# Optimization experiments

Measured on AMD Instinct MI355X. Metric: run time of the kernel, lower is better.

## Reference

```python
import jax, jax.numpy as jnp
import numpy as np

STRIDES = (8, 16, 32)
INPUT = (640, 640)
NC = 80           # num_classes
CONF = 0.65       # conf_thr
IOU_THR = 0.65    # nms iou_threshold
K = 1000          # fixed candidate cap for jit-compatible NMS (padded/masked)


def _priors():
    # MlvlPointGenerator(offset=0, with_stride=True): per level, points at
    # (x*stride, y*stride) flattened y-major, format [cx, cy, stride, stride].
    ps = []
    for s in STRIDES:
        H, W = INPUT[0] // s, INPUT[1] // s
        yy, xx = jnp.meshgrid(jnp.arange(H, dtype=jnp.float32),
                              jnp.arange(W, dtype=jnp.float32), indexing='ij')
        cx = (xx * s).ravel()
        cy = (yy * s).ravel()
        st = jnp.full_like(cx, float(s))
        ps.append(jnp.stack([cx, cy, st, st], axis=-1))
    return jnp.concatenate(ps, axis=0)  # [8400, 4]


def _flatten(xs, c):
    # permute(0,2,3,1).reshape(B, -1, c) per level, concat over priors
    return jnp.concatenate(
        [x.transpose(0, 2, 3, 1).reshape(x.shape[0], -1, c) for x in xs], axis=1)


def _decode(priors, bp):
    # bp: [B, N, 4]; priors: [N, 4] (cx, cy, sw, sh)
    xys = bp[..., :2] * priors[:, 2:] + priors[:, :2]
    whs = jnp.exp(bp[..., 2:]) * priors[:, 2:]
    tl = xys - whs * 0.5
    br = xys + whs * 0.5
    return jnp.concatenate([tl, br], axis=-1)  # [B, N, 4] tlbr


def _iou(a, b):
    tl = jnp.maximum(a[:, None, :2], b[None, :, :2])
    br = jnp.minimum(a[:, None, 2:], b[None, :, 2:])
    wh = jnp.clip(br - tl, 0.0)
    inter = wh[..., 0] * wh[..., 1]
    area = lambda x: (x[:, 2] - x[:, 0]) * (x[:, 3] - x[:, 1])
    union = area(a)[:, None] + area(b)[None, :] - inter
    return inter / (union + 1e-6)


def _nms_single(cls_s, obj_s, boxes):
    # cls_s: [N, NC] sigmoid scores; obj_s: [N]; boxes: [N, 4]
    max_s = cls_s.max(axis=-1)
    labels = jnp.argmax(cls_s, axis=-1)
    score = max_s * obj_s
    valid = score >= CONF                       # confidence mask
    sc = jnp.where(valid, score, 0.0)
    top_sc, idx = jax.lax.top_k(sc, K)          # sorted descending -> greedy order
    b = boxes[idx]
    lab = labels[idx]
    v = valid[idx]
    # class-aware (batched) NMS: offset boxes per label so classes never overlap
    max_coord = jnp.max(jnp.abs(b)) + 1.0
    ob = b + (lab.astype(b.dtype) * max_coord)[:, None]
    iou = _iou(ob, ob)                          # [K, K]
    j = jnp.arange(K)
    def body(i, keep):
        sup = (iou[i] > IOU_THR) & (j > i)
        return jnp.where(keep[i] & v[i], keep & (~sup), keep)
    keep = jax.lax.fori_loop(0, K, body, jnp.ones(K, dtype=bool))
    final = keep & v
    dets = jnp.where(final[:, None],
                     jnp.concatenate([b, top_sc[:, None]], axis=-1), 0.0)  # [K, 5]
    labs = jnp.where(final, lab, -1)
    return dets, labs, final


def setup_inputs() -> dict:
    key = jax.random.key(0)
    ks = jax.random.split(key, 9)
    B = 32
    shapes = {
        'cls0': (B, NC, 80, 80), 'cls1': (B, NC, 40, 40), 'cls2': (B, NC, 20, 20),
        'bbox0': (B, 4, 80, 80), 'bbox1': (B, 4, 40, 40), 'bbox2': (B, 4, 20, 20),
        'obj0': (B, 1, 80, 80), 'obj1': (B, 1, 40, 40), 'obj2': (B, 1, 20, 20),
    }
    return {n: jax.random.normal(k, s, dtype=jnp.float32)
            for (n, s), k in zip(shapes.items(), ks)}


def reference(cls0, cls1, cls2, bbox0, bbox1, bbox2, obj0, obj1, obj2):
    priors = _priors()
    cls = jax.nn.sigmoid(_flatten([cls0, cls1, cls2], NC))       # [B, 8400, 80]
    bp = _flatten([bbox0, bbox1, bbox2], 4)                      # [B, 8400, 4]
    obj = jax.nn.sigmoid(_flatten([obj0, obj1, obj2], 1)[..., 0])  # [B, 8400]
    boxes = _decode(priors, bp)                                  # [B, 8400, 4]
    # per-image class-wise batched NMS, padded to K detections
    dets, labels, keep = jax.vmap(_nms_single)(cls, obj, boxes)
    return dets, labels, keep
```

## Files before the change

### kernel.cpp

```cpp
#include <hip/hip_runtime.h>
#include <stdint.h>

#define NPRIOR 8400
#define NB 32
#define NCLS 80
#define KTOP 1000
#define CAP 8400
#define CPAD 16

typedef unsigned long long u64;

__device__ __forceinline__ float exp_np(float x) {
#pragma clang fp contract(off)
    if (x > 88.72283935546875f) return __builtin_huge_valf();
    if (x < -87.3365478515625f) return 0.0f;
    float q = rintf(x * 1.442695040f);
    float r = fmaf(q, -6.93145752e-1f, x);
    r = fmaf(q, -1.42860677e-6f, r);
    float p = fmaf(1.9875691500e-4f, r, 1.3981999507e-3f);
    p = fmaf(p, r, 8.3334519073e-3f);
    p = fmaf(p, r, 4.1665795894e-2f);
    p = fmaf(p, r, 1.6666665459e-1f);
    p = fmaf(p, r, 5.0000001201e-1f);
    float r2 = r * r;
    p = fmaf(p, r2, r);
    p = p + 1.0f;
    return ldexpf(p, (int)q);
}
__device__ __forceinline__ float sigm_np(float x) {
#pragma clang fp contract(off)
    float t = exp_np(-x);
    return 1.0f / (1.0f + t);
}

__device__ __forceinline__ void level_of(int n, int& W, int& s, int& loc) {
    if (n < 6400)      { W = 80; s = 8;  loc = n; }
    else if (n < 8000) { W = 40; s = 16; loc = n - 6400; }
    else               { W = 20; s = 32; loc = n - 8000; }
}

__device__ float4 decode32(int b, int n,
                           const float* bb0, const float* bb1, const float* bb2) {
#pragma clang fp contract(off)
    int W, s, loc; level_of(n, W, s, loc);
    const float* bb = (s == 8) ? bb0 : (s == 16) ? bb1 : bb2;
    int hw = W * W;
    int y = loc / W, x = loc - y * W;
    const float* bp = bb + (size_t)b * 4 * hw + y * W + x;
    float fs = (float)s;
    float cx = (float)x * fs, cy = (float)y * fs;
    float xc = bp[0] * fs + cx;
    float yc = bp[hw] * fs + cy;
    float wv = exp_np(bp[2 * hw]) * fs;
    float hv = exp_np(bp[3 * hw]) * fs;
    float wv2 = wv * 0.5f, hv2 = hv * 0.5f;
    float4 r;
    r.x = xc - wv2;
    r.y = yc - hv2;
    r.z = xc + wv2;
    r.w = yc + hv2;
    return r;
}

__global__ void __launch_bounds__(64) init_k(int* __restrict__ cnts_mb) {
    cnts_mb[threadIdx.x * CPAD] = 0;
}

__global__ void __launch_bounds__(256) score_k(
    const float* __restrict__ cls0, const float* __restrict__ cls1, const float* __restrict__ cls2,
    const float* __restrict__ ob0,  const float* __restrict__ ob1,  const float* __restrict__ ob2,
    float* __restrict__ sc, int* __restrict__ labels,
    u64* __restrict__ keys, int* __restrict__ cnts, int* __restrict__ rankbuf)
{
#pragma clang fp contract(off)
    int b = blockIdx.y;
    int n = blockIdx.x * 256 + threadIdx.x;
    bool nvalid = (n < NPRIOR);
    int nc = nvalid ? n : NPRIOR - 1;
    int W, s, loc; level_of(nc, W, s, loc);
    const float* cls = (s == 8) ? cls0 : (s == 16) ? cls1 : cls2;
    const float* ob  = (s == 8) ? ob0  : (s == 16) ? ob1  : ob2;
    int hw = W * W;
    int y = loc / W, x = loc - y * W;
    const float* cp = cls + (size_t)b * NCLS * hw + y * W + x;

    float M = -3.4e38f, S2 = -3.4e38f;
    int I = 0;
    for (int cb = 0; cb < NCLS; cb += 8) {
        float buf[8];
#pragma unroll
        for (int k = 0; k < 8; ++k) buf[k] = cp[(size_t)(cb + k) * hw];
#pragma unroll
        for (int k = 0; k < 8; ++k) {
            float l = buf[k];
            if (l > M) { S2 = M; M = l; I = cb + k; }
            else       { S2 = fmaxf(S2, l); }
        }
    }

    float tM = sigm_np(M);
    int lab = I;
    float gap = M - S2;
    float mx = fmaxf(fabsf(M), fabsf(S2));
    if (!((gap * exp_np(-mx)) > 1.6e-5f)) {
        tM = -1.0f; lab = 0;
        for (int c = 0; c < NCLS; ++c) {
            float t = sigm_np(cp[(size_t)c * hw]);
            if (t > tM) { tM = t; lab = c; }
        }
    }
    float sObj = sigm_np(ob[(size_t)b * hw + y * W + x]);
    float score = tM * sObj;
    float scv = (score >= 0.65f) ? score : 0.0f;
    if (nvalid) {
        sc[(size_t)b * NPRIOR + n] = scv;
        labels[(size_t)b * NPRIOR + n] = lab;
    }

    int lane = threadIdx.x & 63;
    bool val = nvalid && (scv > 0.0f);
    u64 mb = __ballot(val);
    if (mb) {
        int lead = (int)__builtin_ctzll(mb);
        int base = 0;
        if (lane == lead) base = atomicAdd(&cnts[b * CPAD], (int)__popcll(mb));
        base = __shfl(base, lead);
        if (val) {
            int pos = base + (int)__popcll(mb & ((1ull << lane) - 1ull));
            keys[(size_t)b * CAP + pos] =
                ((u64)__float_as_uint(scv) << 32) | (unsigned)(~(unsigned)n);
            rankbuf[(size_t)b * CAP + pos] = 0;
        }
    }
}

__global__ void __launch_bounds__(256) rank_part(
    const u64* __restrict__ keys, const int* __restrict__ cnts,
    int* __restrict__ rankbuf)
{
    int b = blockIdx.y, tid = threadIdx.x;
    int cn = min(cnts[b * CPAD], CAP);
    int nt = (cn + 255) >> 8;
    int ntt = nt * nt;
    const u64* keyimg = keys + (size_t)b * CAP;
    int lane = tid & 63;

    for (int t = blockIdx.x; t < ntt; t += gridDim.x) {
        int it = t / nt, jt = t - it * nt;
        int i = it * 256 + tid;
        u64 ki = (i < cn) ? keyimg[i] : ~0ull;
        int rank = 0;
        int jbase = jt * 256;
        int jend = min(jbase + 256, cn);
        for (int jb = jbase; jb < jend; jb += 64) {
            int j = jb + lane;
            u64 kv = (j < cn) ? keyimg[j] : 0ull;
            unsigned lo = (unsigned)kv, hi = (unsigned)(kv >> 32);
            int lim = jend - jb;
#pragma unroll
            for (int l = 0; l < 64; ++l) {
                unsigned jlo = __builtin_amdgcn_readlane(lo, l);
                unsigned jhi = __builtin_amdgcn_readlane(hi, l);
                u64 kj = ((u64)jhi << 32) | jlo;
                rank += (l < lim && kj > ki) ? 1 : 0;
            }
        }
        if (i < cn && rank > 0) atomicAdd(&rankbuf[(size_t)b * CAP + i], rank);
    }
}

__global__ void __launch_bounds__(256) scatter_k(
    const u64* __restrict__ keys, const int* __restrict__ cnts,
    const int* __restrict__ rankbuf,
    const float* __restrict__ sc, const int* __restrict__ labels,
    const float* __restrict__ bb0, const float* __restrict__ bb1, const float* __restrict__ bb2,
    float4* __restrict__ sel_box, float* __restrict__ sel_score,
    int* __restrict__ sel_label, int* __restrict__ maxbits, u64* __restrict__ vmask)
{
#pragma clang fp contract(off)
    __shared__ float redbuf[256];
    int b = blockIdx.y, chunk = blockIdx.x, tid = threadIdx.x;
    int cn = min(cnts[b * CPAD], CAP);
    int base = chunk * 256;
    if (chunk != 0 && base >= cn) return;

    const u64* keyimg = keys + (size_t)b * CAP;
    const int* labb = labels + (size_t)b * NPRIOR;
    const float* scb = sc + (size_t)b * NPRIOR;

    int i = base + tid;
    float lmax = 0.0f;
    if (i < cn) {
        int rank = rankbuf[(size_t)b * CAP + i];
        if (rank < KTOP) {
            u64 ki = keyimg[i];
            unsigned n = ~(unsigned)(ki & 0xffffffffull);
            float s = __uint_as_float((unsigned)(ki >> 32));
            float4 bx = decode32(b, (int)n, bb0, bb1, bb2);
            sel_box[(size_t)b * 1024 + rank] = bx;
            sel_score[(size_t)b * 1024 + rank] = s;
            sel_label[(size_t)b * 1024 + rank] = labb[n];
            lmax = fmaxf(fmaxf(fabsf(bx.x), fabsf(bx.y)),
                         fmaxf(fabsf(bx.z), fabsf(bx.w)));
        }
    }

    if (chunk == 0) {
        if (cn < KTOP && tid == 0) {
            float lm = 0.0f;
            int r = cn;
            for (int n = 0; n < NPRIOR && r < KTOP; ++n) {
                if (scb[n] == 0.0f) {
                    float4 bx = decode32(b, n, bb0, bb1, bb2);
                    sel_box[(size_t)b * 1024 + r] = bx;
                    sel_score[(size_t)b * 1024 + r] = 0.0f;
                    sel_label[(size_t)b * 1024 + r] = labb[n];
                    lm = fmaxf(lm, fmaxf(fmaxf(fabsf(bx.x), fabsf(bx.y)),
                                         fmaxf(fabsf(bx.z), fabsf(bx.w))));
                    ++r;
                }
            }
            lmax = fmaxf(lmax, lm);
        }
        if (tid < 24) {
            sel_box[(size_t)b * 1024 + 1000 + tid] = make_float4(0.f, 0.f, 0.f, 0.f);
            sel_score[(size_t)b * 1024 + 1000 + tid] = 0.0f;
            sel_label[(size_t)b * 1024 + 1000 + tid] = 0;
        }
        if (tid < 16) {
            int vc = min(cn, KTOP);
            int lo = tid * 64;
            u64 m;
            if (vc >= lo + 64)      m = ~0ull;
            else if (vc <= lo)      m = 0ull;
            else                    m = (1ull << (vc - lo)) - 1ull;
            vmask[b * 16 + tid] = m;
        }
    }

    redbuf[tid] = lmax;
    __syncthreads();
    for (int off = 128; off > 0; off >>= 1) {
        if (tid < off) redbuf[tid] = fmaxf(redbuf[tid], redbuf[tid + off]);
        __syncthreads();
    }
    if (tid == 0) atomicMax(&maxbits[b * CPAD], __float_as_int(redbuf[0]));
}

__global__ void __launch_bounds__(256) build_mask_T(
    const float4* __restrict__ sel_box, const int* __restrict__ sel_label,
    const int* __restrict__ maxbits, u64* __restrict__ Cmask)
{
#pragma clang fp contract(off)
    __shared__ float4 obr[256];
    __shared__ float arr[256];
    int b = blockIdx.y;
    int cg = blockIdx.x & 15, rgq = blockIdx.x >> 4;
    if (rgq * 4 > cg) return;
    int tid = threadIdx.x, wave = tid >> 6, lane = tid & 63;
    float mc = __int_as_float(maxbits[b * CPAD]) + 1.0f;

    {
        int row = rgq * 256 + tid;
        float4 v = sel_box[(size_t)b * 1024 + row];
        float off = (float)sel_label[(size_t)b * 1024 + row] * mc;
        v.x += off; v.y += off; v.z += off; v.w += off;
        obr[tid] = v;
        arr[tid] = (v.z - v.x) * (v.w - v.y);
    }
    int col = cg * 64 + lane;
    float4 a = sel_box[(size_t)b * 1024 + col];
    float offc = (float)sel_label[(size_t)b * 1024 + col] * mc;
    a.x += offc; a.y += offc; a.z += offc; a.w += offc;
    float ac = (a.z - a.x) * (a.w - a.y);
    __syncthreads();

    int rg = rgq * 4 + wave;
    if (rg > cg) return;
    u64 bits = 0;
    int rowbase = rg * 64;
#pragma unroll 8
    for (int r = 0; r < 64; ++r) {
        int row = rowbase + r;
        float4 rb = obr[wave * 64 + r];
        float ra = arr[wave * 64 + r];
        bool pred = false;
        if (row < col && row < KTOP && col < KTOP) {
            float tlx = fmaxf(rb.x, a.x), tly = fmaxf(rb.y, a.y);
            float brx = fminf(rb.z, a.z), bry = fminf(rb.w, a.w);
            float w = fmaxf(brx - tlx, 0.0f), h = fmaxf(bry - tly, 0.0f);
            float inter = w * h;
            float uni = (ra + ac) - inter;
            float iou = inter / (uni + 1e-6f);
            pred = iou > 0.65f;
        }
        bits |= pred ? (1ull << r) : 0ull;
    }
    Cmask[((size_t)b * 16 + rg) * 1024 + col] = bits;
}

__global__ void __launch_bounds__(64) nms_fixpoint_write(
    const u64* __restrict__ Cmask, const u64* __restrict__ vmask,
    const float4* __restrict__ sel_box, const float* __restrict__ sel_score,
    const int* __restrict__ sel_label, float* __restrict__ out)
{
    int b = blockIdx.x, lane = threadIdx.x;
    const u64* Cimg = Cmask + (size_t)b * 16 * 1024;
    u64 Khist[16];
#pragma unroll
    for (int g = 0; g < 16; ++g) {
        int col = g * 64 + lane;
        bool supp = false;
#pragma unroll
        for (int gp = 0; gp < g; ++gp)
            supp |= (Cimg[(size_t)gp * 1024 + col] & Khist[gp]) != 0ull;
        u64 V = vmask[b * 16 + g] & ~__ballot(supp);
        u64 T = Cimg[(size_t)g * 1024 + col];
        u64 K = V;
        for (int it = 0; it < 64; ++it) {
            u64 Knew = V & ~__ballot((T & K) != 0ull);
            if (Knew == K) break;
            K = Knew;
        }
        Khist[g] = K;
    }

    const size_t selo = (size_t)b * 1024;
    float* lab_o = out + (size_t)NB * KTOP * 5;
    float* keep_o = lab_o + (size_t)NB * KTOP;
#pragma unroll
    for (int g = 0; g < 16; ++g) {
        int k = g * 64 + lane;
        if (k >= KTOP) break;
        bool fin = (Khist[g] >> lane) & 1ull;
        float4 bx = sel_box[selo + k];
        float s = sel_score[selo + k];
        int lb = sel_label[selo + k];
        size_t o5 = ((size_t)b * KTOP + k) * 5;
        out[o5 + 0] = fin ? bx.x : 0.0f;
        out[o5 + 1] = fin ? bx.y : 0.0f;
        out[o5 + 2] = fin ? bx.z : 0.0f;
        out[o5 + 3] = fin ? bx.w : 0.0f;
        out[o5 + 4] = fin ? s : 0.0f;
        lab_o[b * KTOP + k] = fin ? (float)lb : -1.0f;
        keep_o[b * KTOP + k] = fin ? 1.0f : 0.0f;
    }
}

extern "C" void kernel_launch(void* const* d_in, const int* in_sizes, int n_in,
                              void* d_out, int out_size, void* d_ws, size_t ws_size,
                              hipStream_t stream) {
    const float* cls0 = (const float*)d_in[0];
    const float* cls1 = (const float*)d_in[1];
    const float* cls2 = (const float*)d_in[2];
    const float* bb0  = (const float*)d_in[3];
    const float* bb1  = (const float*)d_in[4];
    const float* bb2  = (const float*)d_in[5];
    const float* ob0  = (const float*)d_in[6];
    const float* ob1  = (const float*)d_in[7];
    const float* ob2  = (const float*)d_in[8];
    float* out = (float*)d_out;

    char* w = (char*)d_ws;
    size_t used = 0;
    auto alloc = [&](size_t bytes) -> void* {
        void* p = (void*)(w + used);
        used += (bytes + 255) & ~(size_t)255;
        return p;
    };
    float* sc        = (float*)alloc((size_t)NB * NPRIOR * 4);
    int* labels      = (int*)alloc((size_t)NB * NPRIOR * 4);
    u64* keys        = (u64*)alloc((size_t)NB * CAP * 8);
    int* cnts_mb     = (int*)alloc((size_t)2 * NB * CPAD * 4);
    int* rankbuf     = (int*)alloc((size_t)NB * CAP * 4);
    float4* sel_box  = (float4*)alloc((size_t)NB * 1024 * 16);
    float* sel_score = (float*)alloc((size_t)NB * 1024 * 4);
    int* sel_label   = (int*)alloc((size_t)NB * 1024 * 4);
    u64* vmask       = (u64*)alloc((size_t)NB * 16 * 8);
    u64* Cmask       = (u64*)alloc((size_t)NB * 16 * 1024 * 8);

    if (used > ws_size) return;

    int* cnts = cnts_mb;
    int* maxbits = cnts_mb + NB * CPAD;

    init_k<<<1, 64, 0, stream>>>(cnts_mb);
    score_k<<<dim3((NPRIOR + 255) / 256, NB), 256, 0, stream>>>(
        cls0, cls1, cls2, ob0, ob1, ob2, sc, labels, keys, cnts, rankbuf);
    rank_part<<<dim3(64, NB), 256, 0, stream>>>(keys, cnts, rankbuf);
    scatter_k<<<dim3((CAP + 255) / 256, NB), 256, 0, stream>>>(
        keys, cnts, rankbuf, sc, labels, bb0, bb1, bb2,
        sel_box, sel_score, sel_label, maxbits, vmask);
    build_mask_T<<<dim3(64, NB), 256, 0, stream>>>(sel_box, sel_label, maxbits, Cmask);
    nms_fixpoint_write<<<NB, 64, 0, stream>>>(
        Cmask, vmask, sel_box, sel_score, sel_label, out);
}
```

Before: 117.8 us.

## Split class max-reduction across 8 channel chunks with a second combine kernel

The per-prior reduction over 80 class logits is split into 8 chunks of 10 classes, each handled by its own block in a first kernel that writes a packed max/index and a second-max to workspace. A second kernel combines the partials, computes the score and does the compaction. The counter reset moves from the separate init kernel into the first kernel. This raises parallelism on the bandwidth-heavy class read (33 blocks x 32 images -> 8x more blocks), at the cost of extra partial-buffer traffic (~25 MB) and one more launch.

```diff
diff --git a/kernel.cpp b/kernel.cpp
--- a/kernel.cpp
+++ b/kernel.cpp
@@ -7,6 +7,8 @@
 #define KTOP 1000
 #define CAP 8400
 #define CPAD 16
+#define PCH 8
+#define CPC 10
 
 typedef unsigned long long u64;
 
@@ -62,47 +64,89 @@
     return r;
 }
 
-__global__ void __launch_bounds__(64) init_k(int* __restrict__ cnts_mb) {
-    cnts_mb[threadIdx.x * CPAD] = 0;
-}
-
-__global__ void __launch_bounds__(256) score_k(
+__device__ __forceinline__ unsigned flt2ord(float f) {
+    unsigned u = __float_as_uint(f);
+    return u ^ ((u >> 31) ? 0xffffffffu : 0x80000000u);
+}
+__device__ __forceinline__ float ord2flt(unsigned u) {
+    u ^= ((u >> 31) ? 0x80000000u : 0xffffffffu);
+    return __uint_as_float(u);
+}
+__device__ __forceinline__ u64 packlc(float l, int c) {
+    return ((u64)flt2ord(l) << 32) | (unsigned)(~(unsigned)c);
+}
+
+__global__ void __launch_bounds__(256) score1_k(
     const float* __restrict__ cls0, const float* __restrict__ cls1, const float* __restrict__ cls2,
-    const float* __restrict__ ob0,  const float* __restrict__ ob1,  const float* __restrict__ ob2,
+    u64* __restrict__ partP, float* __restrict__ partS, int* __restrict__ cnts_mb)
+{
+    int b = blockIdx.z, ch = blockIdx.y;
+    if (blockIdx.x == 0 && ch == 0 && threadIdx.x == 0) {
+        cnts_mb[b * CPAD] = 0;
+        cnts_mb[(NB + b) * CPAD] = 0;
+    }
+    int n = blockIdx.x * 256 + threadIdx.x;
+    if (n >= NPRIOR) return;
+    int W, s, loc; level_of(n, W, s, loc);
+    const float* cls = (s == 8) ? cls0 : (s == 16) ? cls1 : cls2;
+    int hw = W * W;
+    int y = loc / W, x = loc - y * W;
+    const float* cp = cls + (size_t)b * NCLS * hw + (size_t)(ch * CPC) * hw + y * W + x;
+
+    float buf[CPC];
+#pragma unroll
+    for (int k = 0; k < CPC; ++k) buf[k] = cp[(size_t)k * hw];
+    float M = buf[0], S2 = -3.4e38f;
+    int I = ch * CPC;
+#pragma unroll
+    for (int k = 1; k < CPC; ++k) {
+        float l = buf[k];
+        if (l > M) { S2 = M; M = l; I = ch * CPC + k; }
+        else       { S2 = fmaxf(S2, l); }
+    }
+    size_t o = ((size_t)ch * NB + b) * NPRIOR + n;
+    partP[o] = packlc(M, I);
+    partS[o] = S2;
+}
+
+__global__ void __launch_bounds__(256) score2_k(
+    const float* __restrict__ cls0, const float* __restrict__ cls1, const float* __restrict__ cls2,
+    const float* __restrict__ ob0, const float* __restrict__ ob1, const float* __restrict__ ob2,
+    const u64* __restrict__ partP, const float* __restrict__ partS,
     float* __restrict__ sc, int* __restrict__ labels,
     u64* __restrict__ keys, int* __restrict__ cnts, int* __restrict__ rankbuf)
 {
 #pragma clang fp contract(off)
     int b = blockIdx.y;
     int n = blockIdx.x * 256 + threadIdx.x;
-    bool nvalid = (n < NPRIOR);
-    int nc = nvalid ? n : NPRIOR - 1;
-    int W, s, loc; level_of(nc, W, s, loc);
+    if (n >= NPRIOR) return;
+    int W, s, loc; level_of(n, W, s, loc);
     const float* cls = (s == 8) ? cls0 : (s == 16) ? cls1 : cls2;
     const float* ob  = (s == 8) ? ob0  : (s == 16) ? ob1  : ob2;
     int hw = W * W;
     int y = loc / W, x = loc - y * W;
-    const float* cp = cls + (size_t)b * NCLS * hw + y * W + x;
-
-    float M = -3.4e38f, S2 = -3.4e38f;
-    int I = 0;
-    for (int cb = 0; cb < NCLS; cb += 8) {
-        float buf[8];
-#pragma unroll
-        for (int k = 0; k < 8; ++k) buf[k] = cp[(size_t)(cb + k) * hw];
-#pragma unroll
-        for (int k = 0; k < 8; ++k) {
-            float l = buf[k];
-            if (l > M) { S2 = M; M = l; I = cb + k; }
-            else       { S2 = fmaxf(S2, l); }
-        }
-    }
-
+
+    size_t idx = (size_t)b * NPRIOR + n;
+    const size_t cstride = (size_t)NB * NPRIOR;
+    u64 bp = partP[idx];
+    float bz = partS[idx];
+    float m2 = -3.4e38f;
+#pragma unroll
+    for (int ch = 1; ch < PCH; ++ch) {
+        u64 t = partP[(size_t)ch * cstride + idx];
+        float z = partS[(size_t)ch * cstride + idx];
+        if (t > bp) { m2 = fmaxf(m2, ord2flt((unsigned)(bp >> 32))); bp = t; bz = z; }
+        else        { m2 = fmaxf(m2, ord2flt((unsigned)(t >> 32))); }
+    }
+    m2 = fmaxf(m2, bz);
+
+    float M = ord2flt((unsigned)(bp >> 32));
+    int lab = (int)(~(unsigned)(bp & 0xffffffffull));
     float tM = sigm_np(M);
-    int lab = I;
-    float gap = M - S2;
-    float mx = fmaxf(fabsf(M), fabsf(S2));
+    float gap = M - m2;
+    float mx = fmaxf(fabsf(M), fabsf(m2));
     if (!((gap * exp_np(-mx)) > 1.6e-5f)) {
+        const float* cp = cls + (size_t)b * NCLS * hw + y * W + x;
         tM = -1.0f; lab = 0;
         for (int c = 0; c < NCLS; ++c) {
             float t = sigm_np(cp[(size_t)c * hw]);
@@ -112,13 +156,11 @@
     float sObj = sigm_np(ob[(size_t)b * hw + y * W + x]);
     float score = tM * sObj;
     float scv = (score >= 0.65f) ? score : 0.0f;
-    if (nvalid) {
-        sc[(size_t)b * NPRIOR + n] = scv;
-        labels[(size_t)b * NPRIOR + n] = lab;
-    }
+    sc[idx] = scv;
+    labels[idx] = lab;
 
     int lane = threadIdx.x & 63;
-    bool val = nvalid && (scv > 0.0f);
+    bool val = scv > 0.0f;
     u64 mb = __ballot(val);
     if (mb) {
         int lead = (int)__builtin_ctzll(mb);
@@ -370,6 +412,8 @@
     };
     float* sc        = (float*)alloc((size_t)NB * NPRIOR * 4);
     int* labels      = (int*)alloc((size_t)NB * NPRIOR * 4);
+    u64* partP       = (u64*)alloc((size_t)PCH * NB * NPRIOR * 8);
+    float* partS     = (float*)alloc((size_t)PCH * NB * NPRIOR * 4);
     u64* keys        = (u64*)alloc((size_t)NB * CAP * 8);
     int* cnts_mb     = (int*)alloc((size_t)2 * NB * CPAD * 4);
     int* rankbuf     = (int*)alloc((size_t)NB * CAP * 4);
@@ -384,9 +428,11 @@
     int* cnts = cnts_mb;
     int* maxbits = cnts_mb + NB * CPAD;
 
-    init_k<<<1, 64, 0, stream>>>(cnts_mb);
-    score_k<<<dim3((NPRIOR + 255) / 256, NB), 256, 0, stream>>>(
-        cls0, cls1, cls2, ob0, ob1, ob2, sc, labels, keys, cnts, rankbuf);
+    score1_k<<<dim3((NPRIOR + 255) / 256, PCH, NB), 256, 0, stream>>>(
+        cls0, cls1, cls2, partP, partS, cnts_mb);
+    score2_k<<<dim3((NPRIOR + 255) / 256, NB), 256, 0, stream>>>(
+        cls0, cls1, cls2, ob0, ob1, ob2, partP, partS,
+        sc, labels, keys, cnts, rankbuf);
     rank_part<<<dim3(64, NB), 256, 0, stream>>>(keys, cnts, rankbuf);
     scatter_k<<<dim3((CAP + 255) / 256, NB), 256, 0, stream>>>(
         keys, cnts, rankbuf, sc, labels, bb0, bb1, bb2,
```

Measured after the change: 127.0 us. 7.9% more time.

## Split class max-reduction across four lanes per prior with wave shuffles

Applied to the files above, without the earlier changes.

The score kernel now assigns four lanes per prior, each scanning 20 of the 80 class logits. Partial top-1 and runner-up values are merged with xor-shuffles using an order-preserving packed key, so ties resolve to the lowest class index. The goal is more memory-level parallelism and a shorter serial loop in the bandwidth-heavy class scan, which launches four times as many blocks. The cost is only 16 priors per wave, giving narrower contiguous loads per class row, plus extra shuffle work.

```diff
diff --git a/kernel.cpp b/kernel.cpp
--- a/kernel.cpp
+++ b/kernel.cpp
@@ -62,6 +62,18 @@
     return r;
 }
 
+__device__ __forceinline__ unsigned flt2ord(float f) {
+    unsigned u = __float_as_uint(f);
+    return u ^ ((u >> 31) ? 0xffffffffu : 0x80000000u);
+}
+__device__ __forceinline__ float ord2flt(unsigned u) {
+    u ^= ((u >> 31) ? 0x80000000u : 0xffffffffu);
+    return __uint_as_float(u);
+}
+__device__ __forceinline__ u64 packlc(float l, int c) {
+    return ((u64)flt2ord(l) << 32) | (unsigned)(~(unsigned)c);
+}
+
 __global__ void __launch_bounds__(64) init_k(int* __restrict__ cnts_mb) {
     cnts_mb[threadIdx.x * CPAD] = 0;
 }
@@ -74,7 +86,9 @@
 {
 #pragma clang fp contract(off)
     int b = blockIdx.y;
-    int n = blockIdx.x * 256 + threadIdx.x;
+    int tid = threadIdx.x, wv = tid >> 6, l = tid & 63;
+    int cid = l >> 4;
+    int n = blockIdx.x * 64 + wv * 16 + (l & 15);
     bool nvalid = (n < NPRIOR);
     int nc = nvalid ? n : NPRIOR - 1;
     int W, s, loc; level_of(nc, W, s, loc);
@@ -83,50 +97,73 @@
     int hw = W * W;
     int y = loc / W, x = loc - y * W;
     const float* cp = cls + (size_t)b * NCLS * hw + y * W + x;
-
-    float M = -3.4e38f, S2 = -3.4e38f;
-    int I = 0;
-    for (int cb = 0; cb < NCLS; cb += 8) {
-        float buf[8];
-#pragma unroll
-        for (int k = 0; k < 8; ++k) buf[k] = cp[(size_t)(cb + k) * hw];
-#pragma unroll
-        for (int k = 0; k < 8; ++k) {
-            float l = buf[k];
-            if (l > M) { S2 = M; M = l; I = cb + k; }
-            else       { S2 = fmaxf(S2, l); }
-        }
-    }
-
-    float tM = sigm_np(M);
-    int lab = I;
-    float gap = M - S2;
-    float mx = fmaxf(fabsf(M), fabsf(S2));
-    if (!((gap * exp_np(-mx)) > 1.6e-5f)) {
-        tM = -1.0f; lab = 0;
-        for (int c = 0; c < NCLS; ++c) {
-            float t = sigm_np(cp[(size_t)c * hw]);
-            if (t > tM) { tM = t; lab = c; }
-        }
-    }
-    float sObj = sigm_np(ob[(size_t)b * hw + y * W + x]);
-    float score = tM * sObj;
-    float scv = (score >= 0.65f) ? score : 0.0f;
-    if (nvalid) {
+    int c0 = cid * 20;
+
+    float buf[20];
+#pragma unroll
+    for (int k = 0; k < 20; ++k) buf[k] = cp[(size_t)(c0 + k) * hw];
+    float M = buf[0], S2 = -3.4e38f;
+    int I = c0;
+#pragma unroll
+    for (int k = 1; k < 20; ++k) {
+        float lg = buf[k];
+        if (lg > M) { S2 = M; M = lg; I = c0 + k; }
+        else        { S2 = fmaxf(S2, lg); }
+    }
+    u64 p = packlc(M, I);
+    float s2 = S2;
+#pragma unroll
+    for (int mk = 16; mk <= 32; mk <<= 1) {
+        u64 po = __shfl_xor(p, mk, 64);
+        float so = __shfl_xor(s2, mk, 64);
+        if (po > p) { s2 = fmaxf(so, ord2flt((unsigned)(p >> 32))); p = po; }
+        else        { s2 = fmaxf(s2, ord2flt((unsigned)(po >> 32))); }
+    }
+
+    float Mg = ord2flt((unsigned)(p >> 32));
+    int lab = (int)(~(unsigned)(p & 0xffffffffull)) & 0xff;
+    float tM = sigm_np(Mg);
+    float gap = Mg - s2;
+    float mx = fmaxf(fabsf(Mg), fabsf(s2));
+    bool need = !((gap * exp_np(-mx)) > 1.6e-5f) && nvalid;
+    if (__ballot(need)) {
+        u64 pk = 0;
+#pragma unroll
+        for (int k = 0; k < 20; ++k) {
+            float t = sigm_np(cp[(size_t)(c0 + k) * hw]);
+            u64 q = ((u64)flt2ord(t) << 32) | (unsigned)(~(unsigned)(c0 + k));
+            pk = (q > pk) ? q : pk;
+        }
+#pragma unroll
+        for (int mk = 16; mk <= 32; mk <<= 1) {
+            u64 qo = __shfl_xor(pk, mk, 64);
+            pk = (qo > pk) ? qo : pk;
+        }
+        if (need) {
+            tM = ord2flt((unsigned)(pk >> 32));
+            lab = (int)(~(unsigned)(pk & 0xffffffffull)) & 0xff;
+        }
+    }
+
+    bool owner = (cid == 0) && nvalid;
+    float scv = 0.0f;
+    if (owner) {
+        float sObj = sigm_np(ob[(size_t)b * hw + y * W + x]);
+        float score = tM * sObj;
+        scv = (score >= 0.65f) ? score : 0.0f;
         sc[(size_t)b * NPRIOR + n] = scv;
         labels[(size_t)b * NPRIOR + n] = lab;
     }
 
-    int lane = threadIdx.x & 63;
-    bool val = nvalid && (scv > 0.0f);
+    bool val = owner && (scv > 0.0f);
     u64 mb = __ballot(val);
     if (mb) {
         int lead = (int)__builtin_ctzll(mb);
         int base = 0;
-        if (lane == lead) base = atomicAdd(&cnts[b * CPAD], (int)__popcll(mb));
+        if (l == lead) base = atomicAdd(&cnts[b * CPAD], (int)__popcll(mb));
         base = __shfl(base, lead);
         if (val) {
-            int pos = base + (int)__popcll(mb & ((1ull << lane) - 1ull));
+            int pos = base + (int)__popcll(mb & ((1ull << l) - 1ull));
             keys[(size_t)b * CAP + pos] =
                 ((u64)__float_as_uint(scv) << 32) | (unsigned)(~(unsigned)n);
             rankbuf[(size_t)b * CAP + pos] = 0;
@@ -385,7 +422,7 @@
     int* maxbits = cnts_mb + NB * CPAD;
 
     init_k<<<1, 64, 0, stream>>>(cnts_mb);
-    score_k<<<dim3((NPRIOR + 255) / 256, NB), 256, 0, stream>>>(
+    score_k<<<dim3((NPRIOR + 63) / 64, NB), 256, 0, stream>>>(
         cls0, cls1, cls2, ob0, ob1, ob2, sc, labels, keys, cnts, rankbuf);
     rank_part<<<dim3(64, NB), 256, 0, stream>>>(keys, cnts, rankbuf);
     scatter_k<<<dim3((CAP + 255) / 256, NB), 256, 0, stream>>>(
```

Measured after the change: 117.4 us. No clear change (-0.3%).

## Split class argmax across waves with float4 loads and LDS merge

Applied to the files above, without the earlier changes.

The score kernel now has each wave read a 20-class slice for four adjacent priors using float4 loads. Each wave keeps a per-element max and second-max, and the partial results are merged through shared memory as packed ordered keys. This is meant to raise memory-level parallelism and load width for the 80-class scan, which dominates the score pass. It adds LDS traffic and a block barrier, and depends on float4 alignment of groups of four priors within each level.

```diff
diff --git a/kernel.cpp b/kernel.cpp
--- a/kernel.cpp
+++ b/kernel.cpp
@@ -62,19 +62,76 @@
     return r;
 }
 
+__device__ __forceinline__ unsigned flt2ord(float f) {
+    unsigned u = __float_as_uint(f);
+    return u ^ ((u >> 31) ? 0xffffffffu : 0x80000000u);
+}
+__device__ __forceinline__ float ord2flt(unsigned u) {
+    u ^= ((u >> 31) ? 0x80000000u : 0xffffffffu);
+    return __uint_as_float(u);
+}
+__device__ __forceinline__ u64 packlc(float l, int c) {
+    return ((u64)flt2ord(l) << 32) | (unsigned)(~(unsigned)c);
+}
+
 __global__ void __launch_bounds__(64) init_k(int* __restrict__ cnts_mb) {
     cnts_mb[threadIdx.x * CPAD] = 0;
 }
 
-__global__ void __launch_bounds__(256) score_k(
+__global__ void __launch_bounds__(256, 4) score_k(
     const float* __restrict__ cls0, const float* __restrict__ cls1, const float* __restrict__ cls2,
     const float* __restrict__ ob0,  const float* __restrict__ ob1,  const float* __restrict__ ob2,
     float* __restrict__ sc, int* __restrict__ labels,
     u64* __restrict__ keys, int* __restrict__ cnts, int* __restrict__ rankbuf)
 {
 #pragma clang fp contract(off)
+    __shared__ u64 packsLDS[4 * 256];
+    __shared__ float s2LDS[4 * 256];
     int b = blockIdx.y;
-    int n = blockIdx.x * 256 + threadIdx.x;
+    int tid = threadIdx.x, wv = tid >> 6, l = tid & 63;
+
+    {
+        int q = blockIdx.x * 64 + l;
+        int qc = (q < NPRIOR / 4) ? q : NPRIOR / 4 - 1;
+        int n0 = qc * 4;
+        int W, s, loc; level_of(n0, W, s, loc);
+        const float* cls = (s == 8) ? cls0 : (s == 16) ? cls1 : cls2;
+        int hw = W * W;
+        int y = loc / W, x = loc - y * W;
+        const float* cp = cls + (size_t)b * NCLS * hw + y * W + x;
+        int c0 = wv * 20;
+
+        float4 buf[20];
+#pragma unroll
+        for (int k = 0; k < 20; ++k)
+            buf[k] = *(const float4*)(cp + (size_t)(c0 + k) * hw);
+
+        float M[4], S2[4]; int I[4];
+#pragma unroll
+        for (int e = 0; e < 4; ++e) {
+            float v0 = (e == 0) ? buf[0].x : (e == 1) ? buf[0].y
+                     : (e == 2) ? buf[0].z : buf[0].w;
+            M[e] = v0; S2[e] = -3.4e38f; I[e] = c0;
+        }
+#pragma unroll
+        for (int k = 1; k < 20; ++k) {
+#pragma unroll
+            for (int e = 0; e < 4; ++e) {
+                float lg = (e == 0) ? buf[k].x : (e == 1) ? buf[k].y
+                         : (e == 2) ? buf[k].z : buf[k].w;
+                if (lg > M[e]) { S2[e] = M[e]; M[e] = lg; I[e] = c0 + k; }
+                else           { S2[e] = fmaxf(S2[e], lg); }
+            }
+        }
+#pragma unroll
+        for (int e = 0; e < 4; ++e) {
+            packsLDS[wv * 256 + e * 64 + l] = packlc(M[e], I[e]);
+            s2LDS[wv * 256 + e * 64 + l] = S2[e];
+        }
+    }
+    __syncthreads();
+
+    int n = blockIdx.x * 256 + tid;
     bool nvalid = (n < NPRIOR);
     int nc = nvalid ? n : NPRIOR - 1;
     int W, s, loc; level_of(nc, W, s, loc);
@@ -82,42 +139,43 @@
     const float* ob  = (s == 8) ? ob0  : (s == 16) ? ob1  : ob2;
     int hw = W * W;
     int y = loc / W, x = loc - y * W;
-    const float* cp = cls + (size_t)b * NCLS * hw + y * W + x;
-
-    float M = -3.4e38f, S2 = -3.4e38f;
-    int I = 0;
-    for (int cb = 0; cb < NCLS; cb += 8) {
-        float buf[8];
-#pragma unroll
-        for (int k = 0; k < 8; ++k) buf[k] = cp[(size_t)(cb + k) * hw];
-#pragma unroll
-        for (int k = 0; k < 8; ++k) {
-            float l = buf[k];
-            if (l > M) { S2 = M; M = l; I = cb + k; }
-            else       { S2 = fmaxf(S2, l); }
-        }
-    }
-
-    float tM = sigm_np(M);
-    int lab = I;
-    float gap = M - S2;
-    float mx = fmaxf(fabsf(M), fabsf(S2));
-    if (!((gap * exp_np(-mx)) > 1.6e-5f)) {
+
+    int li = (tid & 3) * 64 + (tid >> 2);
+    u64 bp = packsLDS[li];
+    float bz = s2LDS[li];
+    float m2 = -3.4e38f;
+#pragma unroll
+    for (int ch = 1; ch < 4; ++ch) {
+        u64 t = packsLDS[ch * 256 + li];
+        float z = s2LDS[ch * 256 + li];
+        if (t > bp) { m2 = fmaxf(m2, ord2flt((unsigned)(bp >> 32))); bp = t; bz = z; }
+        else        { m2 = fmaxf(m2, ord2flt((unsigned)(t >> 32))); }
+    }
+    m2 = fmaxf(m2, bz);
+
+    float Mg = ord2flt((unsigned)(bp >> 32));
+    int lab = (int)(~(unsigned)(bp & 0xffffffffull)) & 0xff;
+    float tM = sigm_np(Mg);
+    float gap = Mg - m2;
+    float mx = fmaxf(fabsf(Mg), fabsf(m2));
+    if (!((gap * exp_np(-mx)) > 1.6e-5f) && nvalid) {
+        const float* cpe = cls + (size_t)b * NCLS * hw + y * W + x;
         tM = -1.0f; lab = 0;
         for (int c = 0; c < NCLS; ++c) {
-            float t = sigm_np(cp[(size_t)c * hw]);
+            float t = sigm_np(cpe[(size_t)c * hw]);
             if (t > tM) { tM = t; lab = c; }
         }
     }
-    float sObj = sigm_np(ob[(size_t)b * hw + y * W + x]);
-    float score = tM * sObj;
-    float scv = (score >= 0.65f) ? score : 0.0f;
+    float scv = 0.0f;
     if (nvalid) {
+        float sObj = sigm_np(ob[(size_t)b * hw + y * W + x]);
+        float score = tM * sObj;
+        scv = (score >= 0.65f) ? score : 0.0f;
         sc[(size_t)b * NPRIOR + n] = scv;
         labels[(size_t)b * NPRIOR + n] = lab;
     }
 
-    int lane = threadIdx.x & 63;
+    int lane = tid & 63;
     bool val = nvalid && (scv > 0.0f);
     u64 mb = __ballot(val);
     if (mb) {
@@ -385,7 +443,7 @@
     int* maxbits = cnts_mb + NB * CPAD;
 
     init_k<<<1, 64, 0, stream>>>(cnts_mb);
-    score_k<<<dim3((NPRIOR + 255) / 256, NB), 256, 0, stream>>>(
+    score_k<<<dim3((NPRIOR / 4 + 63) / 64, NB), 256, 0, stream>>>(
         cls0, cls1, cls2, ob0, ob1, ob2, sc, labels, keys, cnts, rankbuf);
     rank_part<<<dim3(64, NB), 256, 0, stream>>>(keys, cnts, rankbuf);
     scatter_k<<<dim3((CAP + 255) / 256, NB), 256, 0, stream>>>(
```

After: 120.9 us. 2.7% more time.
